# Kernel tuning notes

Measured on AMD Instinct MI355X. Metric: run time of the kernel, lower is better.

Reference implementation:

```python
import jax, jax.numpy as jnp
import numpy as np

N_NODES = 400_000
N_EDGES = 1_600_000  # reverse-paired: edge 2i and 2i+1 are mutual reverses
N_GRAPHS = 10_000
NODE_DIM, EDGE_DIM, HIDDEN, CONV_LAYERS, TARGET = 74, 13, 64, 4, 1
SLOPE = 0.01  # nn.LeakyReLU() default


def lrelu(x):
    return jax.nn.leaky_relu(x, SLOPE)


def setup_inputs() -> dict:
    key = jax.random.key(0)
    ks = jax.random.split(key, 20)
    half = N_EDGES // 2
    u = jax.random.randint(ks[0], (half,), 0, N_NODES)
    v = jax.random.randint(ks[1], (half,), 0, N_NODES)
    src = jnp.stack([u, v], axis=1).reshape(-1)  # [E]
    dst = jnp.stack([v, u], axis=1).reshape(-1)  # [E]
    node_gid = jnp.sort(jax.random.randint(ks[2], (N_NODES,), 0, N_GRAPHS))

    def lin(k, din, dout):
        kw, kb = jax.random.split(k)
        s = 1.0 / np.sqrt(din)
        return (jax.random.uniform(kw, (din, dout), minval=-s, maxval=s),
                jax.random.uniform(kb, (dout,), minval=-s, maxval=s))

    Wn, bn = lin(ks[3], NODE_DIM, HIDDEN)
    We, be = lin(ks[4], EDGE_DIM, HIDDEN)
    Wi, bi = lin(ks[5], 2 * HIDDEN, HIDDEN)
    Wa, ba = lin(ks[6], 2 * HIDDEN, HIDDEN)
    Wls = []
    for l in range(CONV_LAYERS):
        Wls.append(lin(ks[7 + l], HIDDEN, HIDDEN))
    Wl = jnp.stack([w for w, _ in Wls])  # [L,H,H]
    bl = jnp.stack([b for _, b in Wls])  # [L,H]
    W1, b1 = lin(ks[12], HIDDEN, HIDDEN)
    W2, b2 = lin(ks[13], HIDDEN, TARGET)

    return {
        'node_feats': jax.random.normal(ks[14], (N_NODES, NODE_DIM), jnp.float32),
        'edge_feats': jax.random.normal(ks[15], (N_EDGES, EDGE_DIM), jnp.float32),
        'src': src, 'dst': dst, 'node_gid': node_gid,
        'Wn': Wn, 'bn': bn, 'We': We, 'be': be, 'Wi': Wi, 'bi': bi,
        'Wa': Wa, 'ba': ba, 'Wl': Wl, 'bl': bl,
        'W1': W1, 'b1': b1, 'W2': W2, 'b2': b2,
    }


def reference(node_feats, edge_feats, src, dst, node_gid,
              Wn, bn, We, be, Wi, bi, Wa, ba, Wl, bl, W1, b1, W2, b2):
    E = src.shape[0]
    rev = jnp.arange(E) ^ 1  # reverse-edge index (paired construction)

    node = node_feats @ Wn + bn              # [N,H]
    edge = edge_feats @ We + be              # [E,H]
    h0 = lrelu(jnp.concatenate([node[src], edge], axis=-1) @ Wi + bi)  # [E,H]

    h = h0
    for l in range(CONV_LAYERS):
        # sum of incoming directed-edge states at every node
        agg = jax.ops.segment_sum(h, dst, num_segments=node.shape[0])  # [N,H]
        # DMPNN message: incoming to src(e) excluding the reverse edge
        m = agg[src] - h[rev]                                          # [E,H]
        h = lrelu(h0 + m @ Wl[l] + bl[l])  # dropout = identity (inference)

    # node readout: sum of incoming final edge states
    a = jax.ops.segment_sum(h, dst, num_segments=node.shape[0])        # [N,H]
    node_h = lrelu(jnp.concatenate([node, a], axis=-1) @ Wa + ba)      # [N,H]

    # graph pooling: sum nodes per graph
    g = jax.ops.segment_sum(node_h, node_gid, num_segments=N_GRAPHS)   # [G,H]

    # Linears head (last layer linear, no activation)
    x = lrelu(g @ W1 + b1)
    return x @ W2 + b2                                                 # [G,1]
```

## Files before the change

### kernel.cpp

```cpp
#include <hip/hip_runtime.h>
#include <hip/hip_fp16.h>
#include <stdint.h>

#define N_NODES 400000
#define N_EDGES 1600000
#define N_GRAPHS 10000
#define SLOPE 0.01f

typedef _Float16 hf4 __attribute__((ext_vector_type(4)));
typedef _Float16 hf8 __attribute__((ext_vector_type(8)));
typedef float f32x4 __attribute__((ext_vector_type(4)));

__device__ __forceinline__ float lrelu(float x) { return x > 0.f ? x : SLOPE * x; }

__global__ void k_fold(const float* We, const float* be, const float* Wi, const float* bi,
                       const float* Wn, const float* bn, const float* Wa, const float* ba,
                       const float* Wl, float* WeWi, float* bfold, _Float16* WlT16,
                       _Float16* WTn, float* bnWi, _Float16* WTo, float* bna) {
    int j = threadIdx.x;
    for (int d = 0; d < 13; d++) {
        float acc = 0.f;
        for (int k = 0; k < 64; k++) acc += We[d * 64 + k] * Wi[(64 + k) * 64 + j];
        WeWi[d * 64 + j] = acc;
    }
    float accb = bi[j];
    for (int k = 0; k < 64; k++) accb += be[k] * Wi[(64 + k) * 64 + j];
    bfold[j] = accb;
    for (int l = 0; l < 4; l++)
        for (int k = 0; k < 64; k++)
            WlT16[l * 4096 + j * 64 + k] = (_Float16)Wl[l * 4096 + k * 64 + j];
    for (int d = 0; d < 96; d++) {
        float acc = 0.f;
        if (d < 74)
            for (int k = 0; k < 64; k++) acc += Wn[d * 64 + k] * Wi[k * 64 + j];
        WTn[j * 96 + d] = (_Float16)acc;
    }
    {
        float acc = 0.f;
        for (int k = 0; k < 64; k++) acc += bn[k] * Wi[k * 64 + j];
        bnWi[j] = acc;
    }
    for (int d = 0; d < 160; d++) {
        float acc = 0.f;
        if (d < 74)
            for (int k = 0; k < 64; k++) acc += Wn[d * 64 + k] * Wa[k * 64 + j];
        else if (d >= 80 && d < 144)
            acc = Wa[(64 + d - 80) * 64 + j];
        WTo[j * 160 + d] = (_Float16)acc;
    }
    {
        float acc = ba[j];
        for (int k = 0; k < 64; k++) acc += bn[k] * Wa[k * 64 + j];
        bna[j] = acc;
    }
}

__global__ __launch_bounds__(256) void k_node(const float* nf, const _Float16* WTn,
                                              const float* bnWi, _Float16* nodeWi) {
    __shared__ __align__(16) _Float16 A[64 * 104];
    __shared__ __align__(16) _Float16 WT[64 * 104];
    int t = threadIdx.x;
    int n0 = blockIdx.x * 64;
    for (int idx = t; idx < 64 * 96; idx += 256) {
        int r = idx / 96, c = idx % 96;
        float v = (c < 74) ? nf[(size_t)(n0 + r) * 74 + c] : 0.f;
        A[r * 104 + c] = (_Float16)v;
    }
    for (int idx = t; idx < 64 * 24; idx += 256) {
        int r = idx / 24, c4 = idx % 24;
        *(hf4*)&WT[r * 104 + c4 * 4] = *(const hf4*)(WTn + r * 96 + c4 * 4);
    }
    __syncthreads();
    int lane = t & 63, w = t >> 6;
    int m16 = lane & 15, quad = lane >> 4;
    f32x4 acc[4];
#pragma unroll
    for (int jt = 0; jt < 4; jt++) acc[jt] = (f32x4){0.f, 0.f, 0.f, 0.f};
#pragma unroll
    for (int kt = 0; kt < 3; kt++) {
        hf8 a = *(const hf8*)&A[(w * 16 + m16) * 104 + kt * 32 + quad * 8];
#pragma unroll
        for (int jt = 0; jt < 4; jt++) {
            hf8 b = *(const hf8*)&WT[(jt * 16 + m16) * 104 + kt * 32 + quad * 8];
            acc[jt] = __builtin_amdgcn_mfma_f32_16x16x32_f16(a, b, acc[jt], 0, 0, 0);
        }
    }
#pragma unroll
    for (int jt = 0; jt < 4; jt++) {
        int col = jt * 16 + m16;
        float bb = bnWi[col];
#pragma unroll
        for (int r = 0; r < 4; r++) {
            int row = w * 16 + quad * 4 + r;
            nodeWi[(size_t)(n0 + row) * 64 + col] = (_Float16)(acc[jt][r] + bb);
        }
    }
}

__global__ __launch_bounds__(256) void k_h0(const float* ef, const int* src, const int* dst,
                                            const float* WeWi, const float* bfold,
                                            const _Float16* nodeWi, _Float16* h,
                                            __half2* agg2) {
    __shared__ float efL[832];
    __shared__ float WW[832];
    __shared__ float bf[64];
    __shared__ int dstL[64];
    int t = threadIdx.x;
    int e0 = blockIdx.x * 64;
    int j = t & 63, sub = t >> 6;
    int sv[16];
#pragma unroll
    for (int i = 0; i < 16; i++) sv[i] = src[e0 + sub + 4 * i];
    _Float16 nwv[16];
#pragma unroll
    for (int i = 0; i < 16; i++) nwv[i] = nodeWi[(size_t)sv[i] * 64 + j];
    for (int v = t; v < 832; v += 256) efL[v] = ef[(size_t)e0 * 13 + v];
    for (int v = t; v < 832; v += 256) WW[v] = WeWi[v];
    if (t < 64) { bf[t] = bfold[t]; dstL[t] = dst[e0 + t]; }
    __syncthreads();
    float bfj = bf[j];
#pragma unroll
    for (int i = 0; i < 16; i++) {
        int el = sub + 4 * i;
        int e = e0 + el;
        float acc = bfj + (float)nwv[i];
        const float* er = &efL[el * 13];
#pragma unroll
        for (int d = 0; d < 13; d++) acc += er[d] * WW[d * 64 + j];
        float v = lrelu(acc);
        h[(size_t)e * 64 + j] = (_Float16)v;
        float vn = __shfl_down(v, 1, 64);
        if ((j & 1) == 0) {
            __half2 p = __halves2half2(__float2half(v), __float2half(vn));
            unsafeAtomicAdd(&agg2[(size_t)dstL[el] * 32 + (j >> 1)], p);
        }
    }
}

__global__ __launch_bounds__(256) void k_conv(const _Float16* agg, _Float16* h,
                                              const _Float16* nodeWi, const float* ef,
                                              const int* src, const int* dst,
                                              const float* WeWi, const float* bfold,
                                              const _Float16* WlT16, const float* bl_g,
                                              int layer, __half2* aggN2) {
    __shared__ __align__(16) char uni[18432];
    _Float16* Msh = (_Float16*)uni;
    _Float16* WTs = (_Float16*)(uni + 9216);
    float* Cs = (float*)uni;
    __shared__ float efL[832];
    __shared__ float WWL[832];
    __shared__ float bfL[64];
    __shared__ int dstL[64];
    int t = threadIdx.x;
    int e0 = blockIdx.x * 64;
    int j = t & 63, sub = t >> 6;
    const _Float16* WTg = WlT16 + layer * 4096;
    int sv[16];
#pragma unroll
    for (int i = 0; i < 16; i++) sv[i] = src[e0 + sub + 4 * i];
    _Float16 nwv[16];
#pragma unroll
    for (int i = 0; i < 16; i++) nwv[i] = nodeWi[(size_t)sv[i] * 64 + j];
    for (int i = 0; i < 4; i++) {
        int idx = t + 256 * i;
        int r = idx >> 4, c4 = idx & 15;
        *(hf4*)&WTs[r * 72 + c4 * 4] = *(const hf4*)(WTg + r * 64 + c4 * 4);
    }
    for (int i = 0; i < 4; i++) {
        int idx = t + 256 * i;
        int e = idx >> 4, k4 = idx & 15;
        int ge = e0 + e;
        int s = src[ge];
        hf4 av = *(const hf4*)(agg + (size_t)s * 64 + k4 * 4);
        hf4 hv = *(const hf4*)(h + (size_t)(ge ^ 1) * 64 + k4 * 4);
        hf4 m;
        m.x = av.x - hv.x; m.y = av.y - hv.y; m.z = av.z - hv.z; m.w = av.w - hv.w;
        *(hf4*)&Msh[e * 72 + k4 * 4] = m;
    }
    for (int v = t; v < 832; v += 256) efL[v] = ef[(size_t)e0 * 13 + v];
    for (int v = t; v < 832; v += 256) WWL[v] = WeWi[v];
    if (t < 64) { bfL[t] = bfold[t]; dstL[t] = dst[e0 + t]; }
    __syncthreads();
    int lane = t & 63, w = t >> 6;
    int m16 = lane & 15, quad = lane >> 4;
    f32x4 acc[4];
#pragma unroll
    for (int jt = 0; jt < 4; jt++) acc[jt] = (f32x4){0.f, 0.f, 0.f, 0.f};
#pragma unroll
    for (int kt = 0; kt < 2; kt++) {
        hf8 a = *(const hf8*)&Msh[(w * 16 + m16) * 72 + kt * 32 + quad * 8];
#pragma unroll
        for (int jt = 0; jt < 4; jt++) {
            hf8 b = *(const hf8*)&WTs[(jt * 16 + m16) * 72 + kt * 32 + quad * 8];
            acc[jt] = __builtin_amdgcn_mfma_f32_16x16x32_f16(a, b, acc[jt], 0, 0, 0);
        }
    }
    __syncthreads();
#pragma unroll
    for (int jt = 0; jt < 4; jt++)
#pragma unroll
        for (int r = 0; r < 4; r++)
            Cs[(w * 16 + quad * 4 + r) * 65 + jt * 16 + m16] = acc[jt][r];
    __syncthreads();
    float blj = bl_g[layer * 64 + j];
    float bfj = bfL[j];
#pragma unroll
    for (int i = 0; i < 16; i++) {
        int el = sub + 4 * i;
        int ge = e0 + el;
        float z = bfj + (float)nwv[i];
        const float* er = &efL[el * 13];
#pragma unroll
        for (int d = 0; d < 13; d++) z += er[d] * WWL[d * 64 + j];
        float val = lrelu(lrelu(z) + Cs[el * 65 + j] + blj);
        h[(size_t)ge * 64 + j] = (_Float16)val;
        float vn = __shfl_down(val, 1, 64);
        if ((j & 1) == 0) {
            __half2 p = __halves2half2(__float2half(val), __float2half(vn));
            unsafeAtomicAdd(&aggN2[(size_t)dstL[el] * 32 + (j >> 1)], p);
        }
    }
}

__global__ __launch_bounds__(256) void k_nodeout(const float* nf, const _Float16* agg,
                                                 const _Float16* WTo, const float* bna,
                                                 const int* gidp, float* g) {
    __shared__ __align__(16) char uni[43008];
    _Float16* A = (_Float16*)uni;
    _Float16* WT = (_Float16*)(uni + 21504);
    float* Cs = (float*)uni;
    __shared__ int gidL[64];
    int t = threadIdx.x;
    int n0 = blockIdx.x * 64;
    for (int idx = t; idx < 64 * 80; idx += 256) {
        int r = idx / 80, c = idx % 80;
        float v = (c < 74) ? nf[(size_t)(n0 + r) * 74 + c] : 0.f;
        A[r * 168 + c] = (_Float16)v;
    }
    for (int idx = t; idx < 64 * 16; idx += 256) {
        int r = idx >> 4, c4 = idx & 15;
        *(hf4*)&A[r * 168 + 80 + c4 * 4] = *(const hf4*)(agg + (size_t)(n0 + r) * 64 + c4 * 4);
    }
    for (int idx = t; idx < 64 * 16; idx += 256) {
        int r = idx >> 4, c = idx & 15;
        A[r * 168 + 144 + c] = (_Float16)0.f;
    }
    for (int idx = t; idx < 64 * 40; idx += 256) {
        int r = idx / 40, c4 = idx % 40;
        *(hf4*)&WT[r * 168 + c4 * 4] = *(const hf4*)(WTo + r * 160 + c4 * 4);
    }
    if (t < 64) gidL[t] = gidp[n0 + t];
    __syncthreads();
    int lane = t & 63, w = t >> 6;
    int m16 = lane & 15, quad = lane >> 4;
    f32x4 acc[4];
#pragma unroll
    for (int jt = 0; jt < 4; jt++) acc[jt] = (f32x4){0.f, 0.f, 0.f, 0.f};
#pragma unroll
    for (int kt = 0; kt < 5; kt++) {
        hf8 a = *(const hf8*)&A[(w * 16 + m16) * 168 + kt * 32 + quad * 8];
#pragma unroll
        for (int jt = 0; jt < 4; jt++) {
            hf8 b = *(const hf8*)&WT[(jt * 16 + m16) * 168 + kt * 32 + quad * 8];
            acc[jt] = __builtin_amdgcn_mfma_f32_16x16x32_f16(a, b, acc[jt], 0, 0, 0);
        }
    }
    __syncthreads();
#pragma unroll
    for (int jt = 0; jt < 4; jt++) {
        int col = jt * 16 + m16;
        float bb = bna[col];
#pragma unroll
        for (int r = 0; r < 4; r++) {
            int row = w * 16 + quad * 4 + r;
            Cs[row * 66 + col] = lrelu(acc[jt][r] + bb);
        }
    }
    __syncthreads();
    int jj = t & 63, sub = t >> 6;
    int r0 = sub * 16;
    float run = Cs[r0 * 66 + jj];
    int curg = gidL[r0];
#pragma unroll
    for (int r = r0 + 1; r < r0 + 16; r++) {
        int gg = gidL[r];
        float v = Cs[r * 66 + jj];
        if (gg == curg) {
            run += v;
        } else {
            atomicAdd(&g[(size_t)curg * 64 + jj], run);
            curg = gg;
            run = v;
        }
    }
    atomicAdd(&g[(size_t)curg * 64 + jj], run);
}

__global__ __launch_bounds__(256) void k_head(const float* g, const float* W1,
                                              const float* b1, const float* W2,
                                              const float* b2, float* out) {
    __shared__ float W1L[4096];
    int t = threadIdx.x;
    for (int v = t; v < 4096; v += 256) W1L[v] = W1[v];
    __syncthreads();
    int w = t >> 6, j = t & 63;
    int graph = blockIdx.x * 4 + w;
    if (graph >= N_GRAPHS) return;
    const float* gr = g + (size_t)graph * 64;
    float acc = b1[j];
    for (int k = 0; k < 64; k++) acc += gr[k] * W1L[k * 64 + j];
    float p = lrelu(acc) * W2[j];
    for (int off = 32; off > 0; off >>= 1) p += __shfl_down(p, off, 64);
    if (j == 0) out[graph] = p + b2[0];
}

extern "C" void kernel_launch(void* const* d_in, const int* in_sizes, int n_in,
                              void* d_out, int out_size, void* d_ws, size_t ws_size,
                              hipStream_t stream) {
    const float* nf = (const float*)d_in[0];
    const float* ef = (const float*)d_in[1];
    const int* src = (const int*)d_in[2];
    const int* dst = (const int*)d_in[3];
    const int* gid = (const int*)d_in[4];
    const float* Wn = (const float*)d_in[5];
    const float* bn = (const float*)d_in[6];
    const float* We = (const float*)d_in[7];
    const float* be = (const float*)d_in[8];
    const float* Wi = (const float*)d_in[9];
    const float* bi = (const float*)d_in[10];
    const float* Wa = (const float*)d_in[11];
    const float* ba = (const float*)d_in[12];
    const float* Wl = (const float*)d_in[13];
    const float* bl = (const float*)d_in[14];
    const float* W1 = (const float*)d_in[15];
    const float* b1 = (const float*)d_in[16];
    const float* W2 = (const float*)d_in[17];
    const float* b2 = (const float*)d_in[18];

    char* ws = (char*)d_ws;
    size_t off = 0;
    auto alloc = [&](size_t bytes) -> char* {
        char* p = ws + off;
        off += (bytes + 255) & ~(size_t)255;
        return p;
    };
    float* WeWi = (float*)alloc(13 * 64 * 4);
    float* bfold = (float*)alloc(64 * 4);
    _Float16* WlT16 = (_Float16*)alloc(4 * 4096 * 2);
    _Float16* WTn = (_Float16*)alloc(64 * 96 * 2);
    float* bnWi = (float*)alloc(64 * 4);
    _Float16* WTo = (_Float16*)alloc(64 * 160 * 2);
    float* bna = (float*)alloc(64 * 4);
    _Float16* nodeWi = (_Float16*)alloc((size_t)N_NODES * 64 * 2);
    _Float16* h = (_Float16*)alloc((size_t)N_EDGES * 64 * 2);
    _Float16* aggA = (_Float16*)alloc((size_t)N_NODES * 64 * 2);
    _Float16* aggB = (_Float16*)alloc((size_t)N_NODES * 64 * 2);
    float* g = (float*)alloc((size_t)N_GRAPHS * 64 * 4);

    hipLaunchKernelGGL(k_fold, dim3(1), dim3(64), 0, stream, We, be, Wi, bi, Wn, bn, Wa, ba,
                       Wl, WeWi, bfold, WlT16, WTn, bnWi, WTo, bna);
    hipLaunchKernelGGL(k_node, dim3(N_NODES / 64), dim3(256), 0, stream, nf, WTn, bnWi, nodeWi);
    hipMemsetAsync(aggA, 0, (size_t)N_NODES * 64 * 2, stream);
    hipLaunchKernelGGL(k_h0, dim3(N_EDGES / 64), dim3(256), 0, stream, ef, src, dst, WeWi,
                       bfold, nodeWi, h, (__half2*)aggA);

    _Float16* cur = aggA;
    _Float16* nxt = aggB;
    for (int l = 0; l < 4; l++) {
        hipMemsetAsync(nxt, 0, (size_t)N_NODES * 64 * 2, stream);
        hipLaunchKernelGGL(k_conv, dim3(N_EDGES / 64), dim3(256), 0, stream, cur, h, nodeWi,
                           ef, src, dst, WeWi, bfold, WlT16, bl, l, (__half2*)nxt);
        _Float16* tmp = cur; cur = nxt; nxt = tmp;
    }
    hipMemsetAsync(g, 0, (size_t)N_GRAPHS * 64 * 4, stream);
    hipLaunchKernelGGL(k_nodeout, dim3(N_NODES / 64), dim3(256), 0, stream, nf, cur, WTo, bna,
                       gid, g);
    hipLaunchKernelGGL(k_head, dim3(N_GRAPHS / 4), dim3(256), 0, stream, g, W1, b1, W2, b2,
                       (float*)d_out);
}
```

Baseline: 2.256 ms.

## Compute edge-feature projection with MFMA and fuse epilogue directly from accumulators

The 13-wide edge-feature projection (recomputing h0) moves from scalar FMA loops onto MFMA. The weights are packed as fp16 and zero-padded so that in k_conv the message GEMM and the edge GEMM share one shared-memory B tile. The epilogue now reads straight from MFMA accumulator registers and drops the shared-memory C staging and its extra barriers. Node-projection gathers are rearranged to match the accumulator layout. The trade-offs are lower precision for the edge projection, since features are cast to fp16, and extra padded MFMA work.

```diff
diff --git a/kernel.cpp b/kernel.cpp
--- a/kernel.cpp
+++ b/kernel.cpp
@@ -15,20 +15,25 @@
 
 __global__ void k_fold(const float* We, const float* be, const float* Wi, const float* bi,
                        const float* Wn, const float* bn, const float* Wa, const float* ba,
-                       const float* Wl, float* WeWi, float* bfold, _Float16* WlT16,
+                       const float* Wl, float* bfold, _Float16* WB0, _Float16* WLE,
                        _Float16* WTn, float* bnWi, _Float16* WTo, float* bna) {
     int j = threadIdx.x;
+    float wew[13];
     for (int d = 0; d < 13; d++) {
         float acc = 0.f;
         for (int k = 0; k < 64; k++) acc += We[d * 64 + k] * Wi[(64 + k) * 64 + j];
-        WeWi[d * 64 + j] = acc;
+        wew[d] = acc;
     }
     float accb = bi[j];
     for (int k = 0; k < 64; k++) accb += be[k] * Wi[(64 + k) * 64 + j];
     bfold[j] = accb;
-    for (int l = 0; l < 4; l++)
+    for (int d = 0; d < 40; d++) WB0[j * 40 + d] = (_Float16)((d < 13) ? wew[d] : 0.f);
+    for (int l = 0; l < 4; l++) {
         for (int k = 0; k < 64; k++)
-            WlT16[l * 4096 + j * 64 + k] = (_Float16)Wl[l * 4096 + k * 64 + j];
+            WLE[(l * 64 + j) * 104 + k] = (_Float16)Wl[l * 4096 + k * 64 + j];
+        for (int d = 0; d < 40; d++)
+            WLE[(l * 64 + j) * 104 + 64 + d] = (_Float16)((d < 13) ? wew[d] : 0.f);
+    }
     for (int d = 0; d < 96; d++) {
         float acc = 0.f;
         if (d < 74)
@@ -98,126 +103,165 @@
 }
 
 __global__ __launch_bounds__(256) void k_h0(const float* ef, const int* src, const int* dst,
-                                            const float* WeWi, const float* bfold,
+                                            const _Float16* WB0, const float* bfold,
                                             const _Float16* nodeWi, _Float16* h,
                                             __half2* agg2) {
-    __shared__ float efL[832];
-    __shared__ float WW[832];
-    __shared__ float bf[64];
+    __shared__ __align__(16) _Float16 A[64 * 40];
+    __shared__ __align__(16) _Float16 B[64 * 40];
     __shared__ int dstL[64];
     int t = threadIdx.x;
     int e0 = blockIdx.x * 64;
-    int j = t & 63, sub = t >> 6;
-    int sv[16];
-#pragma unroll
-    for (int i = 0; i < 16; i++) sv[i] = src[e0 + sub + 4 * i];
-    _Float16 nwv[16];
-#pragma unroll
-    for (int i = 0; i < 16; i++) nwv[i] = nodeWi[(size_t)sv[i] * 64 + j];
-    for (int v = t; v < 832; v += 256) efL[v] = ef[(size_t)e0 * 13 + v];
-    for (int v = t; v < 832; v += 256) WW[v] = WeWi[v];
-    if (t < 64) { bf[t] = bfold[t]; dstL[t] = dst[e0 + t]; }
-    __syncthreads();
-    float bfj = bf[j];
-#pragma unroll
-    for (int i = 0; i < 16; i++) {
-        int el = sub + 4 * i;
-        int e = e0 + el;
-        float acc = bfj + (float)nwv[i];
-        const float* er = &efL[el * 13];
-#pragma unroll
-        for (int d = 0; d < 13; d++) acc += er[d] * WW[d * 64 + j];
-        float v = lrelu(acc);
-        h[(size_t)e * 64 + j] = (_Float16)v;
-        float vn = __shfl_down(v, 1, 64);
-        if ((j & 1) == 0) {
-            __half2 p = __halves2half2(__float2half(v), __float2half(vn));
-            unsafeAtomicAdd(&agg2[(size_t)dstL[el] * 32 + (j >> 1)], p);
-        }
-    }
-}
-
-__global__ __launch_bounds__(256) void k_conv(const _Float16* agg, _Float16* h,
-                                              const _Float16* nodeWi, const float* ef,
+    int lane = t & 63, w = t >> 6, m16 = lane & 15, quad = lane >> 4;
+    int rsrc[4];
+#pragma unroll
+    for (int r = 0; r < 4; r++) rsrc[r] = src[e0 + w * 16 + quad * 4 + r];
+    _Float16 nwv[4][4];
+#pragma unroll
+    for (int r = 0; r < 4; r++)
+#pragma unroll
+        for (int jt = 0; jt < 4; jt++)
+            nwv[r][jt] = nodeWi[(size_t)rsrc[r] * 64 + jt * 16 + m16];
+    for (int idx = t; idx < 640; idx += 256) *(hf4*)&B[idx * 4] = *(const hf4*)(WB0 + idx * 4);
+#pragma unroll
+    for (int i = 0; i < 2; i++) {
+        int idx = t + 256 * i;
+        int r = idx >> 3, c4 = idx & 7;
+        hf4 m;
+#pragma unroll
+        for (int q = 0; q < 4; q++) {
+            int d = c4 * 4 + q;
+            m[q] = (_Float16)((d < 13) ? ef[(size_t)(e0 + r) * 13 + d] : 0.f);
+        }
+        *(hf4*)&A[r * 40 + c4 * 4] = m;
+    }
+    if (t < 64) dstL[t] = dst[e0 + t];
+    float bfv[4];
+#pragma unroll
+    for (int jt = 0; jt < 4; jt++) bfv[jt] = bfold[jt * 16 + m16];
+    __syncthreads();
+    f32x4 acc[4];
+#pragma unroll
+    for (int jt = 0; jt < 4; jt++) acc[jt] = (f32x4){0.f, 0.f, 0.f, 0.f};
+    hf8 a = *(const hf8*)&A[(w * 16 + m16) * 40 + quad * 8];
+#pragma unroll
+    for (int jt = 0; jt < 4; jt++) {
+        hf8 b = *(const hf8*)&B[(jt * 16 + m16) * 40 + quad * 8];
+        acc[jt] = __builtin_amdgcn_mfma_f32_16x16x32_f16(a, b, acc[jt], 0, 0, 0);
+    }
+#pragma unroll
+    for (int r = 0; r < 4; r++) {
+        int row = w * 16 + quad * 4 + r;
+        int dn = dstL[row];
+#pragma unroll
+        for (int jt = 0; jt < 4; jt++) {
+            int col = jt * 16 + m16;
+            float z = acc[jt][r] + (float)nwv[r][jt] + bfv[jt];
+            float v = lrelu(z);
+            float vn = __shfl_down(v, 1, 64);
+            if (!(m16 & 1)) {
+                __half2 p = __halves2half2(__float2half(v), __float2half(vn));
+                *(__half2*)&h[(size_t)(e0 + row) * 64 + col] = p;
+                unsafeAtomicAdd(&agg2[(size_t)dn * 32 + (col >> 1)], p);
+            }
+        }
+    }
+}
+
+__global__ __launch_bounds__(256) void k_conv(const _Float16* agg, const _Float16* h_in,
+                                              _Float16* h_out, const float* ef,
                                               const int* src, const int* dst,
-                                              const float* WeWi, const float* bfold,
-                                              const _Float16* WlT16, const float* bl_g,
+                                              const _Float16* nodeWi, const _Float16* WLE,
+                                              const float* bfold, const float* bl_g,
                                               int layer, __half2* aggN2) {
-    __shared__ __align__(16) char uni[18432];
-    _Float16* Msh = (_Float16*)uni;
-    _Float16* WTs = (_Float16*)(uni + 9216);
-    float* Cs = (float*)uni;
-    __shared__ float efL[832];
-    __shared__ float WWL[832];
-    __shared__ float bfL[64];
+    __shared__ __align__(16) _Float16 A[64 * 104];
+    __shared__ __align__(16) _Float16 Bs[64 * 104];
     __shared__ int dstL[64];
     int t = threadIdx.x;
     int e0 = blockIdx.x * 64;
-    int j = t & 63, sub = t >> 6;
-    const _Float16* WTg = WlT16 + layer * 4096;
-    int sv[16];
-#pragma unroll
-    for (int i = 0; i < 16; i++) sv[i] = src[e0 + sub + 4 * i];
-    _Float16 nwv[16];
-#pragma unroll
-    for (int i = 0; i < 16; i++) nwv[i] = nodeWi[(size_t)sv[i] * 64 + j];
+    int lane = t & 63, w = t >> 6, m16 = lane & 15, quad = lane >> 4;
+    const _Float16* Wg = WLE + (size_t)layer * 64 * 104;
+    int rsrc[4];
+#pragma unroll
+    for (int r = 0; r < 4; r++) rsrc[r] = src[e0 + w * 16 + quad * 4 + r];
+    _Float16 nwv[4][4];
+#pragma unroll
+    for (int r = 0; r < 4; r++)
+#pragma unroll
+        for (int jt = 0; jt < 4; jt++)
+            nwv[r][jt] = nodeWi[(size_t)rsrc[r] * 64 + jt * 16 + m16];
+    for (int idx = t; idx < 1664; idx += 256) *(hf4*)&Bs[idx * 4] = *(const hf4*)(Wg + idx * 4);
+#pragma unroll
     for (int i = 0; i < 4; i++) {
         int idx = t + 256 * i;
         int r = idx >> 4, c4 = idx & 15;
-        *(hf4*)&WTs[r * 72 + c4 * 4] = *(const hf4*)(WTg + r * 64 + c4 * 4);
-    }
-    for (int i = 0; i < 4; i++) {
-        int idx = t + 256 * i;
-        int e = idx >> 4, k4 = idx & 15;
-        int ge = e0 + e;
+        int ge = e0 + r;
         int s = src[ge];
-        hf4 av = *(const hf4*)(agg + (size_t)s * 64 + k4 * 4);
-        hf4 hv = *(const hf4*)(h + (size_t)(ge ^ 1) * 64 + k4 * 4);
+        hf4 av = *(const hf4*)(agg + (size_t)s * 64 + c4 * 4);
+        hf4 hv = *(const hf4*)(h_in + (size_t)(ge ^ 1) * 64 + c4 * 4);
         hf4 m;
         m.x = av.x - hv.x; m.y = av.y - hv.y; m.z = av.z - hv.z; m.w = av.w - hv.w;
-        *(hf4*)&Msh[e * 72 + k4 * 4] = m;
-    }
-    for (int v = t; v < 832; v += 256) efL[v] = ef[(size_t)e0 * 13 + v];
-    for (int v = t; v < 832; v += 256) WWL[v] = WeWi[v];
-    if (t < 64) { bfL[t] = bfold[t]; dstL[t] = dst[e0 + t]; }
-    __syncthreads();
-    int lane = t & 63, w = t >> 6;
-    int m16 = lane & 15, quad = lane >> 4;
-    f32x4 acc[4];
-#pragma unroll
-    for (int jt = 0; jt < 4; jt++) acc[jt] = (f32x4){0.f, 0.f, 0.f, 0.f};
+        *(hf4*)&A[r * 104 + c4 * 4] = m;
+    }
+#pragma unroll
+    for (int i = 0; i < 2; i++) {
+        int idx = t + 256 * i;
+        int r = idx >> 3, c4 = idx & 7;
+        hf4 m;
+#pragma unroll
+        for (int q = 0; q < 4; q++) {
+            int d = c4 * 4 + q;
+            m[q] = (_Float16)((d < 13) ? ef[(size_t)(e0 + r) * 13 + d] : 0.f);
+        }
+        *(hf4*)&A[r * 104 + 64 + c4 * 4] = m;
+    }
+    if (t < 64) dstL[t] = dst[e0 + t];
+    float bfv[4], blv[4];
+#pragma unroll
+    for (int jt = 0; jt < 4; jt++) {
+        bfv[jt] = bfold[jt * 16 + m16];
+        blv[jt] = bl_g[layer * 64 + jt * 16 + m16];
+    }
+    __syncthreads();
+    f32x4 acc1[4], acc2[4];
+#pragma unroll
+    for (int jt = 0; jt < 4; jt++) {
+        acc1[jt] = (f32x4){0.f, 0.f, 0.f, 0.f};
+        acc2[jt] = (f32x4){0.f, 0.f, 0.f, 0.f};
+    }
+    const int rowa = (w * 16 + m16) * 104;
 #pragma unroll
     for (int kt = 0; kt < 2; kt++) {
-        hf8 a = *(const hf8*)&Msh[(w * 16 + m16) * 72 + kt * 32 + quad * 8];
-#pragma unroll
-        for (int jt = 0; jt < 4; jt++) {
-            hf8 b = *(const hf8*)&WTs[(jt * 16 + m16) * 72 + kt * 32 + quad * 8];
-            acc[jt] = __builtin_amdgcn_mfma_f32_16x16x32_f16(a, b, acc[jt], 0, 0, 0);
-        }
-    }
-    __syncthreads();
-#pragma unroll
-    for (int jt = 0; jt < 4; jt++)
-#pragma unroll
-        for (int r = 0; r < 4; r++)
-            Cs[(w * 16 + quad * 4 + r) * 65 + jt * 16 + m16] = acc[jt][r];
-    __syncthreads();
-    float blj = bl_g[layer * 64 + j];
-    float bfj = bfL[j];
-#pragma unroll
-    for (int i = 0; i < 16; i++) {
-        int el = sub + 4 * i;
-        int ge = e0 + el;
-        float z = bfj + (float)nwv[i];
-        const float* er = &efL[el * 13];
-#pragma unroll
-        for (int d = 0; d < 13; d++) z += er[d] * WWL[d * 64 + j];
-        float val = lrelu(lrelu(z) + Cs[el * 65 + j] + blj);
-        h[(size_t)ge * 64 + j] = (_Float16)val;
-        float vn = __shfl_down(val, 1, 64);
-        if ((j & 1) == 0) {
-            __half2 p = __halves2half2(__float2half(val), __float2half(vn));
-            unsafeAtomicAdd(&aggN2[(size_t)dstL[el] * 32 + (j >> 1)], p);
+        hf8 a = *(const hf8*)&A[rowa + kt * 32 + quad * 8];
+#pragma unroll
+        for (int jt = 0; jt < 4; jt++) {
+            hf8 b = *(const hf8*)&Bs[(jt * 16 + m16) * 104 + kt * 32 + quad * 8];
+            acc1[jt] = __builtin_amdgcn_mfma_f32_16x16x32_f16(a, b, acc1[jt], 0, 0, 0);
+        }
+    }
+    {
+        hf8 a = *(const hf8*)&A[rowa + 64 + quad * 8];
+#pragma unroll
+        for (int jt = 0; jt < 4; jt++) {
+            hf8 b = *(const hf8*)&Bs[(jt * 16 + m16) * 104 + 64 + quad * 8];
+            acc2[jt] = __builtin_amdgcn_mfma_f32_16x16x32_f16(a, b, acc2[jt], 0, 0, 0);
+        }
+    }
+#pragma unroll
+    for (int r = 0; r < 4; r++) {
+        int row = w * 16 + quad * 4 + r;
+        int dn = dstL[row];
+#pragma unroll
+        for (int jt = 0; jt < 4; jt++) {
+            int col = jt * 16 + m16;
+            float z = acc2[jt][r] + (float)nwv[r][jt] + bfv[jt];
+            float h0v = lrelu(z);
+            float val = lrelu(h0v + acc1[jt][r] + blv[jt]);
+            float vn = __shfl_down(val, 1, 64);
+            if (!(m16 & 1)) {
+                __half2 p = __halves2half2(__float2half(val), __float2half(vn));
+                *(__half2*)&h_out[(size_t)(e0 + row) * 64 + col] = p;
+                unsafeAtomicAdd(&aggN2[(size_t)dn * 32 + (col >> 1)], p);
+            }
         }
     }
 }
@@ -344,9 +388,9 @@
         off += (bytes + 255) & ~(size_t)255;
         return p;
     };
-    float* WeWi = (float*)alloc(13 * 64 * 4);
     float* bfold = (float*)alloc(64 * 4);
-    _Float16* WlT16 = (_Float16*)alloc(4 * 4096 * 2);
+    _Float16* WB0 = (_Float16*)alloc(64 * 40 * 2);
+    _Float16* WLE = (_Float16*)alloc(4 * 64 * 104 * 2);
     _Float16* WTn = (_Float16*)alloc(64 * 96 * 2);
     float* bnWi = (float*)alloc(64 * 4);
     _Float16* WTo = (_Float16*)alloc(64 * 160 * 2);
@@ -358,18 +402,18 @@
     float* g = (float*)alloc((size_t)N_GRAPHS * 64 * 4);
 
     hipLaunchKernelGGL(k_fold, dim3(1), dim3(64), 0, stream, We, be, Wi, bi, Wn, bn, Wa, ba,
-                       Wl, WeWi, bfold, WlT16, WTn, bnWi, WTo, bna);
+                       Wl, bfold, WB0, WLE, WTn, bnWi, WTo, bna);
     hipLaunchKernelGGL(k_node, dim3(N_NODES / 64), dim3(256), 0, stream, nf, WTn, bnWi, nodeWi);
     hipMemsetAsync(aggA, 0, (size_t)N_NODES * 64 * 2, stream);
-    hipLaunchKernelGGL(k_h0, dim3(N_EDGES / 64), dim3(256), 0, stream, ef, src, dst, WeWi,
+    hipLaunchKernelGGL(k_h0, dim3(N_EDGES / 64), dim3(256), 0, stream, ef, src, dst, WB0,
                        bfold, nodeWi, h, (__half2*)aggA);
 
     _Float16* cur = aggA;
     _Float16* nxt = aggB;
     for (int l = 0; l < 4; l++) {
         hipMemsetAsync(nxt, 0, (size_t)N_NODES * 64 * 2, stream);
-        hipLaunchKernelGGL(k_conv, dim3(N_EDGES / 64), dim3(256), 0, stream, cur, h, nodeWi,
-                           ef, src, dst, WeWi, bfold, WlT16, bl, l, (__half2*)nxt);
+        hipLaunchKernelGGL(k_conv, dim3(N_EDGES / 64), dim3(256), 0, stream, cur, h, h, ef,
+                           src, dst, nodeWi, WLE, bfold, bl, l, (__half2*)nxt);
         _Float16* tmp = cur; cur = nxt; nxt = tmp;
     }
     hipMemsetAsync(g, 0, (size_t)N_GRAPHS * 64 * 4, stream);
```

Result: slower. 2.955 ms (+31.0%).

## Cut shared memory in edge kernels, keep per-lane weights in registers, add restrict

Applied to the files above, without the earlier changes.

k_h0 and k_conv stop staging edge features, folded weights, bias and dst indices in shared memory. Each lane now holds its 13 WeWi column weights in registers and reads edge features and dst from global memory with wave-uniform addresses. Each wave now handles a contiguous block of 16 edges, so the first wave index is made uniform with readfirstlane. k_conv stores the MFMA tile transposed so it can be read back as vec4. __restrict__ and launch_bounds(256,8) are added to free LDS, drop barriers and raise occupancy, at the cost of more global scalar loads and register pressure.

```diff
diff --git a/kernel.cpp b/kernel.cpp
--- a/kernel.cpp
+++ b/kernel.cpp
@@ -55,8 +55,10 @@
     }
 }
 
-__global__ __launch_bounds__(256) void k_node(const float* nf, const _Float16* WTn,
-                                              const float* bnWi, _Float16* nodeWi) {
+__global__ __launch_bounds__(256) void k_node(const float* __restrict__ nf,
+                                              const _Float16* __restrict__ WTn,
+                                              const float* __restrict__ bnWi,
+                                              _Float16* __restrict__ nodeWi) {
     __shared__ __align__(16) _Float16 A[64 * 104];
     __shared__ __align__(16) _Float16 WT[64 * 104];
     int t = threadIdx.x;
@@ -97,75 +99,79 @@
     }
 }
 
-__global__ __launch_bounds__(256) void k_h0(const float* ef, const int* src, const int* dst,
-                                            const float* WeWi, const float* bfold,
-                                            const _Float16* nodeWi, _Float16* h,
-                                            __half2* agg2) {
-    __shared__ float efL[832];
-    __shared__ float WW[832];
-    __shared__ float bf[64];
-    __shared__ int dstL[64];
+__global__ __launch_bounds__(256, 8) void k_h0(const float* __restrict__ ef,
+                                               const int* __restrict__ src,
+                                               const int* __restrict__ dst,
+                                               const float* __restrict__ WeWi,
+                                               const float* __restrict__ bfold,
+                                               const _Float16* __restrict__ nodeWi,
+                                               _Float16* __restrict__ h0,
+                                               __half2* __restrict__ agg2) {
     int t = threadIdx.x;
     int e0 = blockIdx.x * 64;
-    int j = t & 63, sub = t >> 6;
-    int sv[16];
-#pragma unroll
-    for (int i = 0; i < 16; i++) sv[i] = src[e0 + sub + 4 * i];
+    int j = t & 63;
+    int su = __builtin_amdgcn_readfirstlane(t >> 6);
     _Float16 nwv[16];
 #pragma unroll
-    for (int i = 0; i < 16; i++) nwv[i] = nodeWi[(size_t)sv[i] * 64 + j];
-    for (int v = t; v < 832; v += 256) efL[v] = ef[(size_t)e0 * 13 + v];
-    for (int v = t; v < 832; v += 256) WW[v] = WeWi[v];
-    if (t < 64) { bf[t] = bfold[t]; dstL[t] = dst[e0 + t]; }
-    __syncthreads();
-    float bfj = bf[j];
-#pragma unroll
     for (int i = 0; i < 16; i++) {
-        int el = sub + 4 * i;
-        int e = e0 + el;
-        float acc = bfj + (float)nwv[i];
-        const float* er = &efL[el * 13];
-#pragma unroll
-        for (int d = 0; d < 13; d++) acc += er[d] * WW[d * 64 + j];
-        float v = lrelu(acc);
-        h[(size_t)e * 64 + j] = (_Float16)v;
+        int s = src[e0 + su * 16 + i];
+        nwv[i] = nodeWi[(size_t)s * 64 + j];
+    }
+    float wwv[13];
+#pragma unroll
+    for (int d = 0; d < 13; d++) wwv[d] = WeWi[d * 64 + j];
+    float bfj = bfold[j];
+#pragma unroll
+    for (int i = 0; i < 16; i++) {
+        int ge = e0 + su * 16 + i;
+        const float* er = ef + (size_t)ge * 13;
+        float z = bfj + (float)nwv[i];
+#pragma unroll
+        for (int d = 0; d < 13; d++) z += er[d] * wwv[d];
+        float v = lrelu(z);
+        h0[(size_t)ge * 64 + j] = (_Float16)v;
         float vn = __shfl_down(v, 1, 64);
+        int dn = dst[ge];
         if ((j & 1) == 0) {
             __half2 p = __halves2half2(__float2half(v), __float2half(vn));
-            unsafeAtomicAdd(&agg2[(size_t)dstL[el] * 32 + (j >> 1)], p);
-        }
-    }
-}
-
-__global__ __launch_bounds__(256) void k_conv(const _Float16* agg, _Float16* h,
-                                              const _Float16* nodeWi, const float* ef,
-                                              const int* src, const int* dst,
-                                              const float* WeWi, const float* bfold,
-                                              const _Float16* WlT16, const float* bl_g,
-                                              int layer, __half2* aggN2) {
+            unsafeAtomicAdd(&agg2[(size_t)dn * 32 + (j >> 1)], p);
+        }
+    }
+}
+
+__global__ __launch_bounds__(256, 8) void k_conv(const _Float16* __restrict__ agg,
+                                                 _Float16* __restrict__ h,
+                                                 const _Float16* __restrict__ nodeWi,
+                                                 const float* __restrict__ ef,
+                                                 const int* __restrict__ src,
+                                                 const int* __restrict__ dst,
+                                                 const _Float16* __restrict__ WlT16,
+                                                 const float* __restrict__ WeWi,
+                                                 const float* __restrict__ bfold,
+                                                 const float* __restrict__ bl_g, int layer,
+                                                 __half2* __restrict__ aggN2) {
     __shared__ __align__(16) char uni[18432];
     _Float16* Msh = (_Float16*)uni;
     _Float16* WTs = (_Float16*)(uni + 9216);
-    float* Cs = (float*)uni;
-    __shared__ float efL[832];
-    __shared__ float WWL[832];
-    __shared__ float bfL[64];
-    __shared__ int dstL[64];
+    float* CsT = (float*)uni;
     int t = threadIdx.x;
     int e0 = blockIdx.x * 64;
-    int j = t & 63, sub = t >> 6;
+    int j = t & 63;
+    int su = __builtin_amdgcn_readfirstlane(t >> 6);
     const _Float16* WTg = WlT16 + layer * 4096;
-    int sv[16];
-#pragma unroll
-    for (int i = 0; i < 16; i++) sv[i] = src[e0 + sub + 4 * i];
     _Float16 nwv[16];
 #pragma unroll
-    for (int i = 0; i < 16; i++) nwv[i] = nodeWi[(size_t)sv[i] * 64 + j];
+    for (int i = 0; i < 16; i++) {
+        int s = src[e0 + su * 16 + i];
+        nwv[i] = nodeWi[(size_t)s * 64 + j];
+    }
+#pragma unroll
     for (int i = 0; i < 4; i++) {
         int idx = t + 256 * i;
         int r = idx >> 4, c4 = idx & 15;
         *(hf4*)&WTs[r * 72 + c4 * 4] = *(const hf4*)(WTg + r * 64 + c4 * 4);
     }
+#pragma unroll
     for (int i = 0; i < 4; i++) {
         int idx = t + 256 * i;
         int e = idx >> 4, k4 = idx & 15;
@@ -177,9 +183,6 @@
         m.x = av.x - hv.x; m.y = av.y - hv.y; m.z = av.z - hv.z; m.w = av.w - hv.w;
         *(hf4*)&Msh[e * 72 + k4 * 4] = m;
     }
-    for (int v = t; v < 832; v += 256) efL[v] = ef[(size_t)e0 * 13 + v];
-    for (int v = t; v < 832; v += 256) WWL[v] = WeWi[v];
-    if (t < 64) { bfL[t] = bfold[t]; dstL[t] = dst[e0 + t]; }
     __syncthreads();
     int lane = t & 63, w = t >> 6;
     int m16 = lane & 15, quad = lane >> 4;
@@ -197,34 +200,45 @@
     }
     __syncthreads();
 #pragma unroll
-    for (int jt = 0; jt < 4; jt++)
-#pragma unroll
-        for (int r = 0; r < 4; r++)
-            Cs[(w * 16 + quad * 4 + r) * 65 + jt * 16 + m16] = acc[jt][r];
-    __syncthreads();
+    for (int jt = 0; jt < 4; jt++) {
+        int col = jt * 16 + m16;
+        *(f32x4*)&CsT[col * 68 + w * 16 + quad * 4] = acc[jt];
+    }
+    __syncthreads();
+    float wwv[13];
+#pragma unroll
+    for (int d = 0; d < 13; d++) wwv[d] = WeWi[d * 64 + j];
+    float bfj = bfold[j];
     float blj = bl_g[layer * 64 + j];
-    float bfj = bfL[j];
-#pragma unroll
-    for (int i = 0; i < 16; i++) {
-        int el = sub + 4 * i;
-        int ge = e0 + el;
-        float z = bfj + (float)nwv[i];
-        const float* er = &efL[el * 13];
-#pragma unroll
-        for (int d = 0; d < 13; d++) z += er[d] * WWL[d * 64 + j];
-        float val = lrelu(lrelu(z) + Cs[el * 65 + j] + blj);
-        h[(size_t)ge * 64 + j] = (_Float16)val;
-        float vn = __shfl_down(val, 1, 64);
-        if ((j & 1) == 0) {
-            __half2 p = __halves2half2(__float2half(val), __float2half(vn));
-            unsafeAtomicAdd(&aggN2[(size_t)dstL[el] * 32 + (j >> 1)], p);
-        }
-    }
-}
-
-__global__ __launch_bounds__(256) void k_nodeout(const float* nf, const _Float16* agg,
-                                                 const _Float16* WTo, const float* bna,
-                                                 const int* gidp, float* g) {
+#pragma unroll
+    for (int c = 0; c < 4; c++) {
+        f32x4 cs = *(const f32x4*)&CsT[j * 68 + su * 16 + c * 4];
+#pragma unroll
+        for (int r = 0; r < 4; r++) {
+            int i = c * 4 + r;
+            int ge = e0 + su * 16 + i;
+            const float* er = ef + (size_t)ge * 13;
+            float z = bfj + (float)nwv[i];
+#pragma unroll
+            for (int d = 0; d < 13; d++) z += er[d] * wwv[d];
+            float val = lrelu(lrelu(z) + cs[r] + blj);
+            h[(size_t)ge * 64 + j] = (_Float16)val;
+            float vn = __shfl_down(val, 1, 64);
+            int dn = dst[ge];
+            if ((j & 1) == 0) {
+                __half2 p = __halves2half2(__float2half(val), __float2half(vn));
+                unsafeAtomicAdd(&aggN2[(size_t)dn * 32 + (j >> 1)], p);
+            }
+        }
+    }
+}
+
+__global__ __launch_bounds__(256) void k_nodeout(const float* __restrict__ nf,
+                                                 const _Float16* __restrict__ agg,
+                                                 const _Float16* __restrict__ WTo,
+                                                 const float* __restrict__ bna,
+                                                 const int* __restrict__ gidp,
+                                                 float* __restrict__ g) {
     __shared__ __align__(16) char uni[43008];
     _Float16* A = (_Float16*)uni;
     _Float16* WT = (_Float16*)(uni + 21504);
@@ -296,9 +310,12 @@
     atomicAdd(&g[(size_t)curg * 64 + jj], run);
 }
 
-__global__ __launch_bounds__(256) void k_head(const float* g, const float* W1,
-                                              const float* b1, const float* W2,
-                                              const float* b2, float* out) {
+__global__ __launch_bounds__(256) void k_head(const float* __restrict__ g,
+                                              const float* __restrict__ W1,
+                                              const float* __restrict__ b1,
+                                              const float* __restrict__ W2,
+                                              const float* __restrict__ b2,
+                                              float* __restrict__ out) {
     __shared__ float W1L[4096];
     int t = threadIdx.x;
     for (int v = t; v < 4096; v += 256) W1L[v] = W1[v];
@@ -369,7 +386,7 @@
     for (int l = 0; l < 4; l++) {
         hipMemsetAsync(nxt, 0, (size_t)N_NODES * 64 * 2, stream);
         hipLaunchKernelGGL(k_conv, dim3(N_EDGES / 64), dim3(256), 0, stream, cur, h, nodeWi,
-                           ef, src, dst, WeWi, bfold, WlT16, bl, l, (__half2*)nxt);
+                           ef, src, dst, WlT16, WeWi, bfold, bl, l, (__half2*)nxt);
         _Float16* tmp = cur; cur = nxt; nxt = tmp;
     }
     hipMemsetAsync(g, 0, (size_t)N_GRAPHS * 64 * 4, stream);
```

Measured after the change: 2.171 ms. 3.8% less time.
